# Performance work log

Measured on AMD Instinct MI355X. Metric: run time of the kernel, lower is better.

## Reference

```python
import jax, jax.numpy as jnp
import numpy as np

B, T, D, H, W = 2, 16, 64, 64, 64
MAX_GROWTH = 0.0  # max_growth_rate init kwarg

def _ln(x, g, b):
    m = x.mean(-1, keepdims=True)
    v = x.var(-1, keepdims=True)
    return (x - m) * jax.lax.rsqrt(v + 1e-5) * g + b

def _pscan(A, X):
    # linear recurrence h_t = A_t*h_{t-1} + X_t via Blelchlo-style associative scan over axis 1
    def comb(l, r):
        a1, x1 = l
        a2, x2 = r
        return a1 * a2, a2 * x1 + x2
    return jax.lax.associative_scan(comb, (A, X), axis=1)[1]

def setup_inputs() -> dict:
    key = jax.random.key(0)
    ks = jax.random.split(key, 20)
    n = lambda k, s, sc=1.0: jax.random.normal(k, s, dtype=jnp.float32) * sc
    inp = dict(
        x_re=n(ks[0], (B, T, D, H, W)), x_im=n(ks[1], (B, T, D, H, W)),
        h_re=n(ks[2], (B * H * W, 1, D)), h_im=n(ks[3], (B * H * W, 1, D)),
        flux_re=n(ks[4], (B, D)), flux_im=n(ks[5], (B, D)),
        dt_seq=0.01 + 0.1 * jax.random.uniform(ks[6], (B, T), dtype=jnp.float32),
        g_s=jnp.ones(2 * D, jnp.float32), b_s=jnp.zeros(2 * D, jnp.float32),
        Wc=n(ks[7], (3, 3, 2 * D, 2 * D), 1.0 / np.sqrt(9 * 2 * D)), bc=jnp.zeros(2 * D, jnp.float32),
        g_t=jnp.ones(2 * D, jnp.float32), b_t=jnp.zeros(2 * D, jnp.float32),
        E_re=n(ks[8], (D, D), 1.0 / np.sqrt(D)), E_im=n(ks[9], (D, D), 1.0 / np.sqrt(D)),
        Dec_re=n(ks[10], (D, D), 1.0 / np.sqrt(D)), Dec_im=n(ks[11], (D, D), 1.0 / np.sqrt(D)),
        lam_flux_raw=jnp.zeros(D, jnp.float32),
        Wsrc_re=n(ks[12], (D, D), 1.0 / np.sqrt(D)), Wsrc_im=n(ks[13], (D, D), 1.0 / np.sqrt(D)),
        w_gate=n(ks[14], (D,)), b_gate=jnp.zeros(D, jnp.float32),
        lam_re_raw=jnp.ones(D, jnp.float32), lam_im=n(ks[15], (D,)),
        W1=n(ks[16], (2 * D, 8 * D), 1.0 / np.sqrt(2 * D)), b1=jnp.zeros(8 * D, jnp.float32),
        W2=n(ks[17], (8 * D, 2 * D), 1.0 / np.sqrt(8 * D)), b2=jnp.zeros(2 * D, jnp.float32),
    )
    return inp

def _forward(x_re, x_im, h_re, h_im, flux_re, flux_im, dt_seq, g_s, b_s, Wc, bc, g_t, b_t,
             E_re, E_im, Dec_re, Dec_im, lam_flux_raw, Wsrc_re, Wsrc_im, w_gate, b_gate,
             lam_re_raw, lam_im, W1, b1, W2, b2):
    # channel-last complex field (B,T,H,W,D)
    x = jnp.moveaxis(x_re, 2, -1) + 1j * jnp.moveaxis(x_im, 2, -1)
    # --- spatial residual branch: LN -> Clifford(= real 2D conv on [re;im] channels) ---
    xr = jnp.concatenate([x.real, x.imag], -1)  # (B,T,H,W,2D)
    xn = _ln(xr, g_s, b_s).reshape(B * T, H, W, 2 * D)
    xs = jax.lax.conv_general_dilated(xn, Wc, (1, 1), 'SAME',
                                      dimension_numbers=('NHWC', 'HWIO', 'NHWC')) + bc
    xs = xs.reshape(B, T, H, W, 2 * D)
    x = x + (xs[..., :D] + 1j * xs[..., D:])
    # --- eigen-basis encode ---
    x_eig = jnp.einsum('bthwd,de->bthwe', x, E_re + 1j * E_im)
    x_mean = x_eig.mean((2, 3))  # (B,T,D)
    # --- flux tracker scan ---
    lam_f = jax.nn.softplus(lam_flux_raw)
    A_flux = jnp.exp(-lam_f * dt_seq[..., None])  # (B,T,D) real decay
    flux = _pscan(A_flux.astype(x_mean.dtype), x_mean * dt_seq[..., None])
    flux = flux + (flux_re + 1j * flux_im)[:, None, :] * jnp.cumprod(A_flux, axis=1)
    source = jnp.einsum('btd,de->bte', flux, Wsrc_re + 1j * Wsrc_im)
    gate = jax.nn.sigmoid(flux.real * w_gate + b_gate)  # real gate in [0,1]
    flux_out = flux[:, -1]
    ge = gate[:, :, None, None, :]
    forcing = x_eig * ge + source[:, :, None, None, :] * (1.0 - ge)
    # --- temporal propagator (exact exponential integrator) ---
    lam = (MAX_GROWTH - jax.nn.softplus(lam_re_raw)) + 1j * lam_im  # Re(lam) <= max_growth_rate
    op_decay = jnp.exp(lam * dt_seq[..., None])            # (B,T,D)
    op_forcing = (op_decay - 1.0) / lam
    u = forcing * op_forcing[:, :, None, None, :]          # (B,T,H,W,D)
    h_prev = (h_re + 1j * h_im).reshape(B, H, W, D)
    u = u.at[:, 0].add(h_prev * op_decay[:, 0][:, None, None, :])
    A_full = jnp.broadcast_to(op_decay[:, :, None, None, :], u.shape)
    u_out = _pscan(A_full, u)                              # (B,T,H,W,D)
    h_out = u_out[:, -1].reshape(B * H * W, 1, D)
    # --- decode + temporal LN/FFN residual ---
    decoded = jnp.einsum('bthwd,de->bthwe', u_out, Dec_re + 1j * Dec_im)
    dn = _ln(jnp.concatenate([decoded.real, decoded.imag], -1), g_t, b_t)
    h1 = jax.nn.gelu(jnp.einsum('bthwc,cf->bthwf', dn, W1) + b1)
    d2 = jnp.einsum('bthwf,fc->bthwc', h1, W2) + b2
    delta = d2[..., :D] + 1j * d2[..., D:]
    z = x + decoded + delta
    return z, h_out, flux_out

def reference(x_re, x_im, h_re, h_im, flux_re, flux_im, dt_seq, g_s, b_s, Wc, bc, g_t, b_t,
              E_re, E_im, Dec_re, Dec_im, lam_flux_raw, Wsrc_re, Wsrc_im, w_gate, b_gate,
              lam_re_raw, lam_im, W1, b1, W2, b2):
    z, h_out, flux_out = _forward(x_re, x_im, h_re, h_im, flux_re, flux_im, dt_seq, g_s, b_s,
                                  Wc, bc, g_t, b_t, E_re, E_im, Dec_re, Dec_im, lam_flux_raw,
                                  Wsrc_re, Wsrc_im, w_gate, b_gate, lam_re_raw, lam_im,
                                  W1, b1, W2, b2)
    # complex outputs returned as real/imag stacked on last axis
    return (jnp.stack([z.real, z.imag], -1),
            jnp.stack([h_out.real, h_out.imag], -1),
            jnp.stack([flux_out.real, flux_out.imag], -1))
```

## Files before the change

### kernel.cpp

```cpp
#include <hip/hip_runtime.h>
#include <hip/hip_bf16.h>


typedef __hip_bfloat16 bf16;
typedef __attribute__((ext_vector_type(8))) short bhalf8;
typedef __attribute__((ext_vector_type(4))) float floatx4;

#define DEV __device__ __forceinline__

DEV float b2f(const bf16 x) { return __bfloat162float(x); }
DEV bf16  f2b(float x)      { return __float2bfloat16(x); }
DEV unsigned short f2bu(float x) { bf16 h = f2b(x); return *(unsigned short*)&h; }
DEV float bu2f(unsigned short u) { unsigned int t = ((unsigned int)u) << 16; return *(float*)&t; }
DEV float softplusf(float x){ return x > 20.f ? x : log1pf(expf(x)); }
DEV float geluf(float x) {
    float th = tanhf(0.7978845608028654f * (x + 0.044715f * x * x * x));
    return 0.5f * x * (1.f + th);
}

static constexpr int B_ = 2, T_ = 16, D_ = 64, HW = 4096;
static constexpr int NPIX = B_ * T_ * HW;
static constexpr long long N1 = (long long)NPIX * 128;

static constexpr long long BUFA  = 0;
static constexpr long long XUBF  = N1;
static constexpr long long DECBF = N1 + N1 / 2;
static constexpr long long XNBF  = 2 * N1;
static constexpr long long XCBF  = 2 * N1 + N1 / 2;
static constexpr long long XMEAN = 3 * N1;
static constexpr long long TABS  = XMEAN + 4096;
static constexpr long long FLAGO = TABS + 14336;
static constexpr long long WCP   = FLAGO + 64;
static constexpr long long W1P   = WCP + 73728;
static constexpr long long W2P   = W1P + 32768;
static constexpr long long WEP   = W2P + 32768;
static constexpr long long WDP   = WEP + 8192;

static constexpr long long ZOUT = 0;
static constexpr long long HOUT = 16777216;
static constexpr long long FOUT = 17825792;

DEV float ld(const void* p, long long i, bool bf) {
    if (bf) return b2f(((const bf16*)p)[i]);
    return ((const float*)p)[i];
}

__global__ void k_detect(const unsigned short* __restrict__ x, float* __restrict__ ws) {
    int lane = threadIdx.x;
    int cnt = 0;
    for (int i = lane; i < 256; i += 64) {
        int e = (x[i] >> 7) & 0xFF;
        cnt += (e >= 100 && e <= 140) ? 1 : 0;
    }
    for (int m = 1; m < 64; m <<= 1) cnt += __shfl_xor(cnt, m, 64);
    if (lane == 0) ws[FLAGO] = (cnt >= 224) ? 1.f : 0.f;
}

__global__ void k_convert(const void* Wc, const void* W1, const void* W2,
                          const void* Er, const void* Ei, const void* Dr, const void* Di,
                          float* ws) {
    bool bf = ws[FLAGO] != 0.f;
    int i = blockIdx.x * 256 + threadIdx.x;
    unsigned short* wcp = (unsigned short*)(ws + WCP);
    unsigned short* w1p = (unsigned short*)(ws + W1P);
    unsigned short* w2p = (unsigned short*)(ws + W2P);
    unsigned short* wep = (unsigned short*)(ws + WEP);
    unsigned short* wdp = (unsigned short*)(ws + WDP);
    if (i < 147456) {
        int j = i & 7, lane = (i >> 3) & 63, nt = (i >> 9) & 7, kc = (i >> 12) & 3, tap = i >> 14;
        int ic = kc * 32 + ((lane >> 4) << 3) + j, oc = nt * 16 + (lane & 15);
        wcp[i] = f2bu(ld(Wc, tap * 16384 + ic * 128 + oc, bf)); return;
    } i -= 147456;
    if (i < 65536) {
        int j = i & 7, lane = (i >> 3) & 63, nt = (i >> 9) & 31, kc = i >> 14;
        int ic = kc * 32 + ((lane >> 4) << 3) + j, oc = nt * 16 + (lane & 15);
        w1p[i] = f2bu(ld(W1, ic * 512 + oc, bf)); return;
    } i -= 65536;
    if (i < 65536) {
        int j = i & 7, lane = (i >> 3) & 63, nt = (i >> 9) & 7, kc = i >> 12;
        int ic = kc * 32 + ((lane >> 4) << 3) + j, oc = nt * 16 + (lane & 15);
        w2p[i] = f2bu(ld(W2, ic * 128 + oc, bf)); return;
    } i -= 65536;
    if (i < 16384) {
        int j = i & 7, lane = (i >> 3) & 63, nt = (i >> 9) & 7, kc = i >> 12;
        int k = kc * 32 + ((lane >> 4) << 3) + j, n = nt * 16 + (lane & 15);
        float v;
        if (k < 64) v = (n < 64) ? ld(Er, k * 64 + n, bf) : ld(Ei, k * 64 + (n - 64), bf);
        else        v = (n < 64) ? -ld(Ei, (k - 64) * 64 + n, bf) : ld(Er, (k - 64) * 64 + (n - 64), bf);
        wep[i] = f2bu(v); return;
    } i -= 16384;
    if (i < 16384) {
        int j = i & 7, lane = (i >> 3) & 63, nt = (i >> 9) & 7, kc = i >> 12;
        int k = kc * 32 + ((lane >> 4) << 3) + j, n = nt * 16 + (lane & 15);
        float v;
        if (k < 64) v = (n < 64) ? ld(Dr, k * 64 + n, bf) : ld(Di, k * 64 + (n - 64), bf);
        else        v = (n < 64) ? -ld(Di, (k - 64) * 64 + n, bf) : ld(Dr, (k - 64) * 64 + (n - 64), bf);
        wdp[i] = f2bu(v); return;
    }
}

__global__ __launch_bounds__(256) void kA_ln(const void* __restrict__ xre,
                                             const void* __restrict__ xim,
                                             const void* __restrict__ gs,
                                             const void* __restrict__ bs,
                                             float* __restrict__ ws) {
    __shared__ unsigned short sr[64][72] __attribute__((aligned(16)));
    __shared__ unsigned short si[64][72] __attribute__((aligned(16)));
    __shared__ float red[2][4][64];
    __shared__ float mv[64], rv[64], gb[256];
    bool bf = ws[FLAGO] != 0.f;
    int blk = blockIdx.x;
    int bt = blk >> 6;
    int px0 = (blk & 63) * 64;
    int tid = threadIdx.x;
    gb[tid] = (tid < 128) ? ld(gs, tid, bf) : ld(bs, tid - 128, bf);
    if (bf) {
        const unsigned short* xr16 = (const unsigned short*)xre;
        const unsigned short* xi16 = (const unsigned short*)xim;
        for (int l = tid; l < 1024; l += 256) {
            int a = l >> 9, dd = (l >> 3) & 63, ck = l & 7;
            long long src = (long long)bt * 262144 + (long long)dd * 4096 + px0 + ck * 8;
            bhalf8 v = *(const bhalf8*)&(a ? xi16 : xr16)[src];
            *(bhalf8*)&(a ? si : sr)[dd][ck * 8] = v;
        }
    } else {
        for (int l = tid; l < 8192; l += 256) {
            int a = l >> 12, dd = (l >> 6) & 63, px = l & 63;
            float v = ((const float*)(a ? xim : xre))[(long long)bt * 262144 + (long long)dd * 4096 + px0 + px];
            (a ? si : sr)[dd][px] = f2bu(v);
        }
    }
    __syncthreads();
    int px = tid & 63, part = tid >> 6;
    float s = 0.f, ss = 0.f;
    for (int d = part * 16; d < part * 16 + 16; d++) {
        float r = bu2f(sr[d][px]), q = bu2f(si[d][px]);
        s += r + q; ss += r * r + q * q;
    }
    red[0][part][px] = s; red[1][part][px] = ss;
    __syncthreads();
    if (tid < 64) {
        float S  = red[0][0][tid] + red[0][1][tid] + red[0][2][tid] + red[0][3][tid];
        float SS = red[1][0][tid] + red[1][1][tid] + red[1][2][tid] + red[1][3][tid];
        float m = S * (1.f / 128.f);
        mv[tid] = m;
        rv[tid] = rsqrtf(SS * (1.f / 128.f) - m * m + 1e-5f);
    }
    __syncthreads();
    unsigned short* xcb = (unsigned short*)(ws + XCBF);
    unsigned short* xnb = (unsigned short*)(ws + XNBF);
    long long pbase = ((long long)bt * 4096 + px0) * 128;
    for (int l = tid; l < 8192; l += 256) {
        int p2 = l >> 7, ch = l & 127, d = ch & 63;
        unsigned short raw = (ch < 64 ? sr : si)[d][p2];
        float v = bu2f(raw);
        xcb[pbase + p2 * 128 + ch] = raw;
        xnb[pbase + p2 * 128 + ch] = f2bu((v - mv[p2]) * rv[p2] * gb[ch] + gb[128 + ch]);
    }
}

__global__ __launch_bounds__(256) void kB_conv(const void* __restrict__ bc,
                                               float* __restrict__ ws) {
    __shared__ unsigned short xt[3][64][136] __attribute__((aligned(16)));
    bool bf = ws[FLAGO] != 0.f;
    int blk = blockIdx.x, bt = blk >> 6, h = blk & 63;
    int tid = threadIdx.x, lane = tid & 63, wv = tid >> 6;
    int m16 = lane & 15, quad = lane >> 4;
    const unsigned short* xnb = (const unsigned short*)(ws + XNBF);
    const unsigned short* wcp = (const unsigned short*)(ws + WCP);
    bhalf8 zero8 = {0, 0, 0, 0, 0, 0, 0, 0};
    for (int l = tid; l < 3072; l += 256) {
        int r = l >> 10, rem = l & 1023, col = rem >> 4, ck = rem & 15;
        int hr = h - 1 + r;
        bhalf8 v = zero8;
        if (hr >= 0 && hr < 64)
            v = *(const bhalf8*)&xnb[(((long long)bt * 4096 + hr * 64 + col) << 7) + ck * 8];
        *(bhalf8*)&xt[r][col][ck * 8] = v;
    }
    __syncthreads();
    floatx4 acc[4][2];
    #pragma unroll
    for (int mt = 0; mt < 4; mt++)
        #pragma unroll
        for (int nt = 0; nt < 2; nt++)
            acc[mt][nt] = (floatx4){0.f, 0.f, 0.f, 0.f};
    for (int tap = 0; tap < 9; tap++) {
        int dy = tap / 3, dx = tap - dy * 3;
        #pragma unroll
        for (int kc = 0; kc < 4; kc++) {
            bhalf8 bfr[2];
            #pragma unroll
            for (int nt = 0; nt < 2; nt++)
                bfr[nt] = *(const bhalf8*)&wcp[((((tap * 4 + kc) * 8) + (wv * 2 + nt)) * 64 + lane) * 8];
            #pragma unroll
            for (int mt = 0; mt < 4; mt++) {
                int col = mt * 16 + m16 + dx - 1;
                bhalf8 af = zero8;
                if (col >= 0 && col < 64)
                    af = *(const bhalf8*)&xt[dy][col][kc * 32 + quad * 8];
                acc[mt][0] = __builtin_amdgcn_mfma_f32_16x16x32_bf16(af, bfr[0], acc[mt][0], 0, 0, 0);
                acc[mt][1] = __builtin_amdgcn_mfma_f32_16x16x32_bf16(af, bfr[1], acc[mt][1], 0, 0, 0);
            }
        }
    }
    const unsigned short* xcb = (const unsigned short*)(ws + XCBF);
    unsigned short* xub = (unsigned short*)(ws + XUBF);
    #pragma unroll
    for (int nt = 0; nt < 2; nt++) {
        int n = wv * 32 + nt * 16 + m16;
        float bcv = ld(bc, n, bf);
        #pragma unroll
        for (int mt = 0; mt < 4; mt++)
            #pragma unroll
            for (int r = 0; r < 4; r++) {
                int m = mt * 16 + quad * 4 + r;
                long long p = (long long)bt * 4096 + h * 64 + m;
                xub[p * 128 + n] = f2bu(acc[mt][nt][r] + bu2f(xcb[p * 128 + n]) + bcv);
            }
    }
}

__global__ __launch_bounds__(256) void kC_eig(float* __restrict__ ws) {
    __shared__ unsigned short At[64][136] __attribute__((aligned(16)));
    int blk = blockIdx.x, bt = blk >> 6;
    long long px0 = (long long)blk * 64;
    int tid = threadIdx.x, lane = tid & 63, wv = tid >> 6;
    int m16 = lane & 15, quad = lane >> 4;
    const unsigned short* xub = (const unsigned short*)(ws + XUBF);
    for (int l = tid; l < 1024; l += 256) {
        int p2 = l >> 4, ck = l & 15;
        *(bhalf8*)&At[p2][ck * 8] = *(const bhalf8*)&xub[(px0 + p2) * 128 + ck * 8];
    }
    __syncthreads();
    const unsigned short* wep = (const unsigned short*)(ws + WEP);
    floatx4 acc[4][2];
    #pragma unroll
    for (int mt = 0; mt < 4; mt++)
        #pragma unroll
        for (int nt = 0; nt < 2; nt++)
            acc[mt][nt] = (floatx4){0.f, 0.f, 0.f, 0.f};
    #pragma unroll
    for (int kc = 0; kc < 4; kc++) {
        bhalf8 bfr[2];
        #pragma unroll
        for (int nt = 0; nt < 2; nt++)
            bfr[nt] = *(const bhalf8*)&wep[(((kc * 8) + wv * 2 + nt) * 64 + lane) * 8];
        #pragma unroll
        for (int mt = 0; mt < 4; mt++) {
            bhalf8 af = *(const bhalf8*)&At[mt * 16 + m16][kc * 32 + quad * 8];
            acc[mt][0] = __builtin_amdgcn_mfma_f32_16x16x32_bf16(af, bfr[0], acc[mt][0], 0, 0, 0);
            acc[mt][1] = __builtin_amdgcn_mfma_f32_16x16x32_bf16(af, bfr[1], acc[mt][1], 0, 0, 0);
        }
    }
    #pragma unroll
    for (int nt = 0; nt < 2; nt++) {
        int n = wv * 32 + nt * 16 + m16;
        float part = 0.f;
        #pragma unroll
        for (int mt = 0; mt < 4; mt++)
            #pragma unroll
            for (int r = 0; r < 4; r++) {
                int m = mt * 16 + quad * 4 + r;
                ws[BUFA + (px0 + m) * 128 + n] = acc[mt][nt][r];
                part += acc[mt][nt][r];
            }
        part += __shfl_xor(part, 16, 64);
        part += __shfl_xor(part, 32, 64);
        if (quad == 0) atomicAdd(ws + XMEAN + bt * 128 + n, part);
    }
}

__global__ __launch_bounds__(256) void kD_flux(const void* __restrict__ fxr, const void* __restrict__ fxi,
                                               const void* __restrict__ dtseq, const void* __restrict__ lamflux,
                                               const void* __restrict__ Wsr, const void* __restrict__ Wsi,
                                               const void* __restrict__ wgate, const void* __restrict__ bgate,
                                               const void* __restrict__ lamreraw, const void* __restrict__ lamim,
                                               float* __restrict__ ws, void* __restrict__ outv) {
    bool bfo = ws[FLAGO] != 0.f;
    int b = blockIdx.x;
    int tid = threadIdx.x;
    int d = tid & 63, g = tid >> 6;
    __shared__ float fr[64], fi[64], psr[4][64], psi[4][64];
    float lam_f = softplusf(ld(lamflux, d, bfo));
    float lre = -softplusf(ld(lamreraw, d, bfo));
    float lim = ld(lamim, d, bfo);
    float cr = 0.f, ci = 0.f;
    if (g == 0) { cr = ld(fxr, b * 64 + d, bfo); ci = ld(fxi, b * 64 + d, bfo); }
    float* tabs = ws + TABS;
    const float* xmean = ws + XMEAN;
    for (int t = 0; t < 16; t++) {
        float dt = ld(dtseq, b * 16 + t, bfo);
        int idx = b * 1024 + t * 64 + d;
        if (g == 0) {
            float A = expf(-lam_f * dt);
            float xr = xmean[(b * 16 + t) * 128 + d]      * (1.f / 4096.f) * dt;
            float xq = xmean[(b * 16 + t) * 128 + 64 + d] * (1.f / 4096.f) * dt;
            cr = A * cr + xr; ci = A * ci + xq;
            fr[d] = cr; fi[d] = ci;
        }
        __syncthreads();
        {
            float pr = 0.f, pi = 0.f;
            #pragma unroll
            for (int k = 0; k < 16; k++) {
                int d2 = g * 16 + k;
                float wr = ld(Wsr, d2 * 64 + d, bfo), wi = ld(Wsi, d2 * 64 + d, bfo);
                pr += fr[d2] * wr - fi[d2] * wi;
                pi += fr[d2] * wi + fi[d2] * wr;
            }
            psr[g][d] = pr; psi[g][d] = pi;
        }
        if (g == 1) {
            float od  = expf(lre * dt);
            float odr = od * cosf(lim * dt);
            float odi = od * sinf(lim * dt);
            tabs[3 * 2048 + idx] = odr; tabs[4 * 2048 + idx] = odi;
            float den = lre * lre + lim * lim;
            float tr = odr - 1.f;
            tabs[5 * 2048 + idx] = (tr * lre + odi * lim) / den;
            tabs[6 * 2048 + idx] = (odi * lre - tr * lim) / den;
        }
        __syncthreads();
        if (g == 0) {
            float sr = psr[0][d] + psr[1][d] + psr[2][d] + psr[3][d];
            float si2 = psi[0][d] + psi[1][d] + psi[2][d] + psi[3][d];
            tabs[1 * 2048 + idx] = sr; tabs[2 * 2048 + idx] = si2;
            tabs[0 * 2048 + idx] = 1.f / (1.f + expf(-(cr * ld(wgate, d, bfo) + ld(bgate, d, bfo))));
            if (t == 15) {
                if (bfo) {
                    bf16* ob = (bf16*)outv;
                    ob[FOUT + (b * 64 + d) * 2]     = f2b(cr);
                    ob[FOUT + (b * 64 + d) * 2 + 1] = f2b(ci);
                } else {
                    float* of = (float*)outv;
                    of[FOUT + (b * 64 + d) * 2]     = cr;
                    of[FOUT + (b * 64 + d) * 2 + 1] = ci;
                }
            }
        }
    }
}

__global__ __launch_bounds__(256) void kE_scan(const void* __restrict__ hre,
                                               const void* __restrict__ him,
                                               float* __restrict__ ws, void* __restrict__ outv) {
    __shared__ float tab[7][16][64];
    bool bfo = ws[FLAGO] != 0.f;
    long long G = (long long)blockIdx.x * 256 + threadIdx.x;
    int d = threadIdx.x & 63;
    int pix = (int)((G >> 6) & 4095);
    int b = (int)(G >> 18);
    const float* tabs = ws + TABS;
    for (int l = threadIdx.x; l < 7 * 1024; l += 256) {
        int a = l >> 10, idx = l & 1023;
        ((float*)tab)[l] = tabs[a * 2048 + b * 1024 + idx];
    }
    __syncthreads();
    long long hidx = ((long long)b * 4096 + pix) * 64 + d;
    float cr = ld(hre, hidx, bfo), ci = ld(him, hidx, bfo);
    float* xe = ws + BUFA;
    for (int t = 0; t < 16; t++) {
        long long base = ((long long)((b * 16 + t) * 4096 + pix)) * 128 + d;
        float xr = xe[base], xi = xe[base + 64];
        float gt = tab[0][t][d], sr = tab[1][t][d], si = tab[2][t][d];
        float odr = tab[3][t][d], odi = tab[4][t][d];
        float ofr = tab[5][t][d], ofi = tab[6][t][d];
        float fre = xr * gt + sr * (1.f - gt);
        float fim = xi * gt + si * (1.f - gt);
        float ure = fre * ofr - fim * ofi;
        float uim = fre * ofi + fim * ofr;
        float ncr = odr * cr - odi * ci + ure;
        float nci = odr * ci + odi * cr + uim;
        cr = ncr; ci = nci;
        xe[base] = cr; xe[base + 64] = ci;
    }
    if (bfo) {
        __hip_bfloat162 hv; hv.x = f2b(cr); hv.y = f2b(ci);
        ((__hip_bfloat162*)((bf16*)outv + HOUT))[hidx] = hv;
    } else {
        float2 hv; hv.x = cr; hv.y = ci;
        ((float2*)((float*)outv + HOUT))[hidx] = hv;
    }
}

__global__ __launch_bounds__(256) void kF1_dec(const void* __restrict__ gt_,
                                               const void* __restrict__ bt_,
                                               float* __restrict__ ws) {
    __shared__ unsigned short At[64][136] __attribute__((aligned(16)));
    __shared__ float Ct[64][132];
    __shared__ float mv[64], rv[64], gbt[256];
    bool bf = ws[FLAGO] != 0.f;
    long long px0 = (long long)blockIdx.x * 64;
    int tid = threadIdx.x, lane = tid & 63, wv = tid >> 6;
    int m16 = lane & 15, quad = lane >> 4;
    gbt[tid] = (tid < 128) ? ld(gt_, tid, bf) : ld(bt_, tid - 128, bf);
    const float* uo = ws + BUFA + px0 * 128;
    for (int l = tid; l < 2048; l += 256) {
        int p2 = l >> 5, c4 = (l & 31) * 4;
        float4 v = *(const float4*)&uo[p2 * 128 + c4];
        unsigned short* dst = &At[p2][c4];
        dst[0] = f2bu(v.x); dst[1] = f2bu(v.y); dst[2] = f2bu(v.z); dst[3] = f2bu(v.w);
    }
    __syncthreads();
    const unsigned short* wdp = (const unsigned short*)(ws + WDP);
    floatx4 acc[4][2];
    #pragma unroll
    for (int mt = 0; mt < 4; mt++)
        #pragma unroll
        for (int nt = 0; nt < 2; nt++)
            acc[mt][nt] = (floatx4){0.f, 0.f, 0.f, 0.f};
    #pragma unroll
    for (int kc = 0; kc < 4; kc++) {
        bhalf8 bfr[2];
        #pragma unroll
        for (int nt = 0; nt < 2; nt++)
            bfr[nt] = *(const bhalf8*)&wdp[(((kc * 8) + wv * 2 + nt) * 64 + lane) * 8];
        #pragma unroll
        for (int mt = 0; mt < 4; mt++) {
            bhalf8 af = *(const bhalf8*)&At[mt * 16 + m16][kc * 32 + quad * 8];
            acc[mt][0] = __builtin_amdgcn_mfma_f32_16x16x32_bf16(af, bfr[0], acc[mt][0], 0, 0, 0);
            acc[mt][1] = __builtin_amdgcn_mfma_f32_16x16x32_bf16(af, bfr[1], acc[mt][1], 0, 0, 0);
        }
    }
    #pragma unroll
    for (int nt = 0; nt < 2; nt++) {
        int n = wv * 32 + nt * 16 + m16;
        #pragma unroll
        for (int mt = 0; mt < 4; mt++)
            #pragma unroll
            for (int r = 0; r < 4; r++)
                Ct[mt * 16 + quad * 4 + r][n] = acc[mt][nt][r];
    }
    __syncthreads();
    if (tid < 64) {
        float s = 0.f, ss = 0.f;
        for (int ch = 0; ch < 128; ch++) { float v = Ct[tid][ch]; s += v; ss += v * v; }
        float m = s * (1.f / 128.f);
        mv[tid] = m;
        rv[tid] = rsqrtf(ss * (1.f / 128.f) - m * m + 1e-5f);
    }
    __syncthreads();
    unsigned short* decb = (unsigned short*)(ws + DECBF);
    unsigned short* dnb  = (unsigned short*)(ws + XNBF);
    for (int l = tid; l < 8192; l += 256) {
        int p2 = l >> 7, ch = l & 127;
        float v = Ct[p2][ch];
        decb[(px0 + p2) * 128 + ch] = f2bu(v);
        dnb [(px0 + p2) * 128 + ch] = f2bu((v - mv[p2]) * rv[p2] * gbt[ch] + gbt[128 + ch]);
    }
}

__global__ __launch_bounds__(256) void kMLP(const void* __restrict__ b1v,
                                            const void* __restrict__ b2v,
                                            float* __restrict__ ws, void* __restrict__ outv) {
    __shared__ unsigned short A1[32][136] __attribute__((aligned(16)));
    __shared__ unsigned short h1[32][520] __attribute__((aligned(16)));
    bool bf = ws[FLAGO] != 0.f;
    long long px0 = (long long)blockIdx.x * 32;
    int tid = threadIdx.x, lane = tid & 63, wv = tid >> 6;
    int m16 = lane & 15, quad = lane >> 4;
    const unsigned short* dnb = (const unsigned short*)(ws + XNBF);
    for (int l = tid; l < 512; l += 256) {
        int p2 = l >> 4, ck = l & 15;
        *(bhalf8*)&A1[p2][ck * 8] = *(const bhalf8*)&dnb[(px0 + p2) * 128 + ck * 8];
    }
    __syncthreads();
    const unsigned short* w1p = (const unsigned short*)(ws + W1P);
    floatx4 acc1[2][8];
    #pragma unroll
    for (int mt = 0; mt < 2; mt++)
        #pragma unroll
        for (int nt = 0; nt < 8; nt++)
            acc1[mt][nt] = (floatx4){0.f, 0.f, 0.f, 0.f};
    #pragma unroll
    for (int kc = 0; kc < 4; kc++) {
        bhalf8 af0 = *(const bhalf8*)&A1[m16][kc * 32 + quad * 8];
        bhalf8 af1 = *(const bhalf8*)&A1[16 + m16][kc * 32 + quad * 8];
        #pragma unroll
        for (int nt = 0; nt < 8; nt++) {
            bhalf8 bfr = *(const bhalf8*)&w1p[(((kc * 32) + wv * 8 + nt) * 64 + lane) * 8];
            acc1[0][nt] = __builtin_amdgcn_mfma_f32_16x16x32_bf16(af0, bfr, acc1[0][nt], 0, 0, 0);
            acc1[1][nt] = __builtin_amdgcn_mfma_f32_16x16x32_bf16(af1, bfr, acc1[1][nt], 0, 0, 0);
        }
    }
    #pragma unroll
    for (int nt = 0; nt < 8; nt++) {
        int n = (wv * 8 + nt) * 16 + m16;
        float b1f = ld(b1v, n, bf);
        #pragma unroll
        for (int mt = 0; mt < 2; mt++)
            #pragma unroll
            for (int r = 0; r < 4; r++)
                h1[mt * 16 + quad * 4 + r][n] = f2bu(geluf(acc1[mt][nt][r] + b1f));
    }
    __syncthreads();
    const unsigned short* w2p = (const unsigned short*)(ws + W2P);
    floatx4 acc2[2][2];
    #pragma unroll
    for (int mt = 0; mt < 2; mt++)
        #pragma unroll
        for (int nt = 0; nt < 2; nt++)
            acc2[mt][nt] = (floatx4){0.f, 0.f, 0.f, 0.f};
    for (int kc = 0; kc < 16; kc++) {
        bhalf8 af0 = *(const bhalf8*)&h1[m16][kc * 32 + quad * 8];
        bhalf8 af1 = *(const bhalf8*)&h1[16 + m16][kc * 32 + quad * 8];
        #pragma unroll
        for (int nt = 0; nt < 2; nt++) {
            bhalf8 bfr = *(const bhalf8*)&w2p[(((kc * 8) + wv * 2 + nt) * 64 + lane) * 8];
            acc2[0][nt] = __builtin_amdgcn_mfma_f32_16x16x32_bf16(af0, bfr, acc2[0][nt], 0, 0, 0);
            acc2[1][nt] = __builtin_amdgcn_mfma_f32_16x16x32_bf16(af1, bfr, acc2[1][nt], 0, 0, 0);
        }
    }
    const unsigned short* decb = (const unsigned short*)(ws + DECBF);
    const unsigned short* xub  = (const unsigned short*)(ws + XUBF);
    #pragma unroll
    for (int nt = 0; nt < 2; nt++) {
        int n = wv * 32 + nt * 16 + m16;
        float b2f_ = ld(b2v, n, bf);
        #pragma unroll
        for (int mt = 0; mt < 2; mt++)
            #pragma unroll
            for (int r = 0; r < 4; r++) {
                long long p = px0 + mt * 16 + quad * 4 + r;
                float val = acc2[mt][nt][r] + b2f_ + bu2f(xub[p * 128 + n]) + bu2f(decb[p * 128 + n]);
                long long oidx = p * 128 + ((n < 64) ? (2 * n) : (2 * (n - 64) + 1));
                if (bf) ((bf16*)outv)[ZOUT + oidx] = f2b(val);
                else    ((float*)outv)[ZOUT + oidx] = val;
            }
    }
}

extern "C" void kernel_launch(void* const* d_in, const int* in_sizes, int n_in,
                              void* d_out, int out_size, void* d_ws, size_t ws_size,
                              hipStream_t stream) {
    const void* x_re  = d_in[0];
    const void* x_im  = d_in[1];
    const void* h_re  = d_in[2];
    const void* h_im  = d_in[3];
    const void* fl_re = d_in[4];
    const void* fl_im = d_in[5];
    const void* dtseq = d_in[6];
    const void* g_s   = d_in[7];
    const void* b_s   = d_in[8];
    const void* Wc    = d_in[9];
    const void* bc    = d_in[10];
    const void* g_t   = d_in[11];
    const void* b_t   = d_in[12];
    const void* E_re  = d_in[13];
    const void* E_im  = d_in[14];
    const void* De_re = d_in[15];
    const void* De_im = d_in[16];
    const void* lamfl = d_in[17];
    const void* Ws_re = d_in[18];
    const void* Ws_im = d_in[19];
    const void* wgate = d_in[20];
    const void* bgate = d_in[21];
    const void* lamrr = d_in[22];
    const void* lamim = d_in[23];
    const void* W1    = d_in[24];
    const void* b1    = d_in[25];
    const void* W2    = d_in[26];
    const void* b2    = d_in[27];
    float* ws = (float*)d_ws;

    hipMemsetAsync((char*)d_ws + XMEAN * sizeof(float), 0, 4096 * sizeof(float), stream);
    k_detect<<<1, 64, 0, stream>>>((const unsigned short*)x_re, ws);
    k_convert<<<1216, 256, 0, stream>>>(Wc, W1, W2, E_re, E_im, De_re, De_im, ws);
    kA_ln<<<2048, 256, 0, stream>>>(x_re, x_im, g_s, b_s, ws);
    kB_conv<<<2048, 256, 0, stream>>>(bc, ws);
    kC_eig<<<2048, 256, 0, stream>>>(ws);
    kD_flux<<<2, 256, 0, stream>>>(fl_re, fl_im, dtseq, lamfl, Ws_re, Ws_im,
                                   wgate, bgate, lamrr, lamim, ws, d_out);
    kE_scan<<<2048, 256, 0, stream>>>(h_re, h_im, ws, d_out);
    kF1_dec<<<2048, 256, 0, stream>>>(g_t, b_t, ws);
    kMLP<<<4096, 256, 0, stream>>>(b1, b2, ws, d_out);
}
```

Baseline: 512.3 us.

## Store scan intermediates in bf16, vectorize MLP epilogue, use exp-based GELU

The projected inputs and the scan outputs are now stored as bf16 instead of fp32, with the scan writing to a separate buffer. This roughly halves the workspace traffic of the encoder, scan and decoder stages and lets the decoder load its tile with 16-byte vector copies. The MLP epilogue stages its results through shared memory so each thread does vectorized loads of the residuals and writes interleaved real/imag outputs contiguously. GELU is rewritten in sigmoid form with a fast exp and reciprocal. The cost is extra bf16 rounding of intermediates, including the scan state written out each step.

Result: faster. 455.2 us (-11.1%).

```diff
diff --git a/kernel.cpp b/kernel.cpp
--- a/kernel.cpp
+++ b/kernel.cpp
@@ -14,8 +14,9 @@
 DEV float bu2f(unsigned short u) { unsigned int t = ((unsigned int)u) << 16; return *(float*)&t; }
 DEV float softplusf(float x){ return x > 20.f ? x : log1pf(expf(x)); }
 DEV float geluf(float x) {
-    float th = tanhf(0.7978845608028654f * (x + 0.044715f * x * x * x));
-    return 0.5f * x * (1.f + th);
+    float v = x * fmaf(x * x, 0.0713548162726f, 1.5957691216057308f);
+    float e = __expf(-v);
+    return x * __builtin_amdgcn_rcpf(1.f + e);
 }
 
 static constexpr int B_ = 2, T_ = 16, D_ = 64, HW = 4096;
@@ -252,6 +253,7 @@
             acc[mt][1] = __builtin_amdgcn_mfma_f32_16x16x32_bf16(af, bfr[1], acc[mt][1], 0, 0, 0);
         }
     }
+    unsigned short* xeb = (unsigned short*)(ws + BUFA);
     #pragma unroll
     for (int nt = 0; nt < 2; nt++) {
         int n = wv * 32 + nt * 16 + m16;
@@ -261,7 +263,7 @@
             #pragma unroll
             for (int r = 0; r < 4; r++) {
                 int m = mt * 16 + quad * 4 + r;
-                ws[BUFA + (px0 + m) * 128 + n] = acc[mt][nt][r];
+                xeb[(px0 + m) * 128 + n] = f2bu(acc[mt][nt][r]);
                 part += acc[mt][nt][r];
             }
         part += __shfl_xor(part, 16, 64);
@@ -358,10 +360,11 @@
     __syncthreads();
     long long hidx = ((long long)b * 4096 + pix) * 64 + d;
     float cr = ld(hre, hidx, bfo), ci = ld(him, hidx, bfo);
-    float* xe = ws + BUFA;
+    const unsigned short* xe = (const unsigned short*)(ws + BUFA);
+    unsigned short* ub = (unsigned short*)(ws + XCBF);
     for (int t = 0; t < 16; t++) {
         long long base = ((long long)((b * 16 + t) * 4096 + pix)) * 128 + d;
-        float xr = xe[base], xi = xe[base + 64];
+        float xr = bu2f(xe[base]), xi = bu2f(xe[base + 64]);
         float gt = tab[0][t][d], sr = tab[1][t][d], si = tab[2][t][d];
         float odr = tab[3][t][d], odi = tab[4][t][d];
         float ofr = tab[5][t][d], ofi = tab[6][t][d];
@@ -372,7 +375,7 @@
         float ncr = odr * cr - odi * ci + ure;
         float nci = odr * ci + odi * cr + uim;
         cr = ncr; ci = nci;
-        xe[base] = cr; xe[base + 64] = ci;
+        ub[base] = f2bu(cr); ub[base + 64] = f2bu(ci);
     }
     if (bfo) {
         __hip_bfloat162 hv; hv.x = f2b(cr); hv.y = f2b(ci);
@@ -394,12 +397,10 @@
     int tid = threadIdx.x, lane = tid & 63, wv = tid >> 6;
     int m16 = lane & 15, quad = lane >> 4;
     gbt[tid] = (tid < 128) ? ld(gt_, tid, bf) : ld(bt_, tid - 128, bf);
-    const float* uo = ws + BUFA + px0 * 128;
-    for (int l = tid; l < 2048; l += 256) {
-        int p2 = l >> 5, c4 = (l & 31) * 4;
-        float4 v = *(const float4*)&uo[p2 * 128 + c4];
-        unsigned short* dst = &At[p2][c4];
-        dst[0] = f2bu(v.x); dst[1] = f2bu(v.y); dst[2] = f2bu(v.z); dst[3] = f2bu(v.w);
+    const unsigned short* uo = (const unsigned short*)(ws + XCBF);
+    for (int l = tid; l < 1024; l += 256) {
+        int p2 = l >> 4, ck = l & 15;
+        *(bhalf8*)&At[p2][ck * 8] = *(const bhalf8*)&uo[(px0 + p2) * 128 + ck * 8];
     }
     __syncthreads();
     const unsigned short* wdp = (const unsigned short*)(ws + WDP);
@@ -455,11 +456,13 @@
                                             float* __restrict__ ws, void* __restrict__ outv) {
     __shared__ unsigned short A1[32][136] __attribute__((aligned(16)));
     __shared__ unsigned short h1[32][520] __attribute__((aligned(16)));
+    __shared__ float gb2[128];
     bool bf = ws[FLAGO] != 0.f;
     long long px0 = (long long)blockIdx.x * 32;
     int tid = threadIdx.x, lane = tid & 63, wv = tid >> 6;
     int m16 = lane & 15, quad = lane >> 4;
     const unsigned short* dnb = (const unsigned short*)(ws + XNBF);
+    if (tid < 128) gb2[tid] = ld(b2v, tid, bf);
     for (int l = tid; l < 512; l += 256) {
         int p2 = l >> 4, ck = l & 15;
         *(bhalf8*)&A1[p2][ck * 8] = *(const bhalf8*)&dnb[(px0 + p2) * 128 + ck * 8];
@@ -511,22 +514,48 @@
             acc2[1][nt] = __builtin_amdgcn_mfma_f32_16x16x32_bf16(af1, bfr, acc2[1][nt], 0, 0, 0);
         }
     }
-    const unsigned short* decb = (const unsigned short*)(ws + DECBF);
-    const unsigned short* xub  = (const unsigned short*)(ws + XUBF);
+    __syncthreads();
     #pragma unroll
     for (int nt = 0; nt < 2; nt++) {
         int n = wv * 32 + nt * 16 + m16;
-        float b2f_ = ld(b2v, n, bf);
         #pragma unroll
         for (int mt = 0; mt < 2; mt++)
             #pragma unroll
-            for (int r = 0; r < 4; r++) {
-                long long p = px0 + mt * 16 + quad * 4 + r;
-                float val = acc2[mt][nt][r] + b2f_ + bu2f(xub[p * 128 + n]) + bu2f(decb[p * 128 + n]);
-                long long oidx = p * 128 + ((n < 64) ? (2 * n) : (2 * (n - 64) + 1));
-                if (bf) ((bf16*)outv)[ZOUT + oidx] = f2b(val);
-                else    ((float*)outv)[ZOUT + oidx] = val;
-            }
+            for (int r = 0; r < 4; r++)
+                A1[mt * 16 + quad * 4 + r][n] = f2bu(acc2[mt][nt][r]);
+    }
+    __syncthreads();
+    {
+        const unsigned short* decb = (const unsigned short*)(ws + DECBF);
+        const unsigned short* xub  = (const unsigned short*)(ws + XUBF);
+        int pxl = tid >> 3, dc = (tid & 7) * 8;
+        long long p = px0 + pxl;
+        bhalf8 cre = *(const bhalf8*)&A1[pxl][dc];
+        bhalf8 cim = *(const bhalf8*)&A1[pxl][64 + dc];
+        bhalf8 xr8 = *(const bhalf8*)&xub[p * 128 + dc];
+        bhalf8 xi8 = *(const bhalf8*)&xub[p * 128 + 64 + dc];
+        bhalf8 dr8 = *(const bhalf8*)&decb[p * 128 + dc];
+        bhalf8 di8 = *(const bhalf8*)&decb[p * 128 + 64 + dc];
+        float zr[8], zi[8];
+        #pragma unroll
+        for (int k = 0; k < 8; k++) {
+            zr[k] = bu2f((unsigned short)cre[k]) + gb2[dc + k]
+                  + bu2f((unsigned short)xr8[k]) + bu2f((unsigned short)dr8[k]);
+            zi[k] = bu2f((unsigned short)cim[k]) + gb2[64 + dc + k]
+                  + bu2f((unsigned short)xi8[k]) + bu2f((unsigned short)di8[k]);
+        }
+        if (bf) {
+            unsigned short o[16];
+            #pragma unroll
+            for (int k = 0; k < 8; k++) { o[2 * k] = f2bu(zr[k]); o[2 * k + 1] = f2bu(zi[k]); }
+            unsigned short* ob = (unsigned short*)outv;
+            *(bhalf8*)&ob[ZOUT + p * 128 + 2 * dc]     = *(bhalf8*)&o[0];
+            *(bhalf8*)&ob[ZOUT + p * 128 + 2 * dc + 8] = *(bhalf8*)&o[8];
+        } else {
+            float* of = (float*)outv + ZOUT + p * 128 + 2 * dc;
+            #pragma unroll
+            for (int k = 0; k < 8; k++) { of[2 * k] = zr[k]; of[2 * k + 1] = zi[k]; }
+        }
     }
 }
 
```
